# Performance work log

Measured on AMD Instinct MI355X. Metric: run time of the kernel, lower is better.

The kernel has to match this reference:

```python
import jax, jax.numpy as jnp
import numpy as np
import math

B, S, SIG, EMB, LAT, H, L_ENC, L_DEC = 16, 1024, 256, 256, 256, 8, 2, 2
EH, DH = EMB // H, LAT // H
EPS = 1e-10


def _sinusoidal_last_row(d):
    # last row of a standard sinusoidal PE table (position index = max_len-1)
    pos = 5000.0 - 1.0
    i = np.arange(d)
    angles = pos / np.power(10000.0, (2 * (i // 2)) / d)
    pe = np.where(i % 2 == 0, np.sin(angles), np.cos(angles))
    return jnp.asarray(pe, dtype=jnp.float32)


def setup_inputs() -> dict:
    key = jax.random.key(0)
    ks = iter(jax.random.split(key, 64))
    w = lambda *sh: 0.05 * jax.random.normal(next(ks), sh, dtype=jnp.float32)
    z = lambda *sh: jnp.zeros(sh, dtype=jnp.float32)
    d = {
        'inputData': jax.random.normal(next(ks), (B, S, SIG), dtype=jnp.float32),
        'pos_enc': _sinusoidal_last_row(SIG),
        'embW': w(SIG, EMB), 'embb': z(EMB),
        'qW': w(EMB, EMB), 'qb': z(EMB),
        'kW': w(EMB, EMB), 'kb': z(EMB),
        'vW': w(EMB, EMB), 'vb': z(EMB),
        'encBW': w(EH, EH), 'encBb': z(EH),
        'oW': w(EMB, EMB), 'ob': z(EMB),
        'ffe_W1': w(EMB, 2 * EMB), 'ffe_b1': z(2 * EMB),
        'ffe_W2': w(2 * EMB, EMB), 'ffe_b2': z(EMB),
        'lnSA_g': jnp.ones((L_ENC, EMB)), 'lnSA_b': z(L_ENC, EMB),
        'lnFF_g': jnp.ones((L_ENC, EMB)), 'lnFF_b': z(L_ENC, EMB),
        'start': w(1, LAT),
        'decQW': w(LAT, LAT), 'decQb': z(LAT),
        'decKW': w(EMB, EMB), 'decKb': z(EMB),
        'decVW': w(EMB, LAT), 'decVb': z(LAT),
        'decBW': w(EH + DH, DH), 'decBb': z(DH),
        'latW': w(LAT, LAT), 'latb': z(LAT),
        'ffd_W1': w(LAT, LAT // 2), 'ffd_b1': z(LAT // 2),
        'ffd_W2': w(LAT // 2, LAT), 'ffd_b2': z(LAT),
        'lnCA_g': jnp.ones((L_DEC, LAT)), 'lnCA_b': z(L_DEC, LAT),
        'lnLFF_g': jnp.ones((L_DEC, LAT)), 'lnLFF_b': z(L_DEC, LAT),
        'finW': w(LAT, LAT), 'finb': z(LAT),
    }
    return d


def _ln(x, g, b):
    m = x.mean(-1, keepdims=True)
    v = x.var(-1, keepdims=True)
    return (x - m) * jax.lax.rsqrt(v + EPS) * g + b


def _enc_attn(x, qW, qb, kW, kb, vW, vb, bW, bb, oW, ob):
    # x: (B,S,EMB) -> heads (B,H,S,EH)
    sp = lambda t: t.reshape(B, S, H, EH).transpose(0, 2, 1, 3)
    q, k, v = sp(x @ qW + qb), sp(x @ kW + kb), sp(x @ vW + vb)
    bk = k @ bW + bb                                   # bilinear key (B,H,S,EH)
    attn = jax.nn.softmax(jnp.einsum('bhqd,bhkd->bhqk', q, bk) / math.sqrt(EH), axis=-1)
    out = jnp.einsum('bhqk,bhkd->bhqd', attn, v)
    out = out.transpose(0, 2, 1, 3).reshape(B, S, EMB)
    return out @ oW + ob


def _dec_attn(enc, lat, qW, qb, kW, kb, vW, vb, bW, bb, oW, ob):
    # lat: (B,LAT) single query token; enc: (B,S,EMB)
    q = (lat @ qW + qb).reshape(B, 1, H, DH).transpose(0, 2, 1, 3)   # (B,H,1,DH)
    k = (enc @ kW + kb).reshape(B, S, H, EH).transpose(0, 2, 1, 3)   # (B,H,S,EH)
    v = (enc @ vW + vb).reshape(B, S, H, DH).transpose(0, 2, 1, 3)   # (B,H,S,DH)
    qcat = jnp.broadcast_to(q, (B, H, S, DH))
    kcat = jnp.concatenate([k, qcat], axis=-1)                       # (B,H,S,EH+DH)
    bk = kcat @ bW + bb                                              # (B,H,S,DH)
    attn = jax.nn.softmax(jnp.einsum('bhqd,bhkd->bhqk', q, bk) / math.sqrt(EH + DH), axis=-1)
    out = jnp.einsum('bhqk,bhkd->bhqd', attn, v)                     # (B,H,1,DH)
    out = out.transpose(0, 2, 1, 3).reshape(B, LAT)
    return out @ oW + ob


def reference(inputData, pos_enc, embW, embb, qW, qb, kW, kb, vW, vb, encBW, encBb,
              oW, ob, ffe_W1, ffe_b1, ffe_W2, ffe_b2, lnSA_g, lnSA_b, lnFF_g, lnFF_b,
              start, decQW, decQb, decKW, decKb, decVW, decVb, decBW, decBb,
              latW, latb, ffd_W1, ffd_b1, ffd_W2, ffd_b2, lnCA_g, lnCA_b,
              lnLFF_g, lnLFF_b, finW, finb):
    emb = (inputData + pos_enc) @ embW + embb          # (B,S,EMB)
    t = emb
    for l in range(L_ENC):
        n = _ln(t, lnSA_g[l], lnSA_b[l])
        a = _enc_attn(n, qW, qb, kW, kb, vW, vb, encBW, encBb, oW, ob) + n
        t = a + emb
        n2 = _ln(t, lnFF_g[l], lnFF_b[l])
        ff = jax.nn.selu(n2 @ ffe_W1 + ffe_b1) @ ffe_W2 + ffe_b2
        t = ff + n2
    init_lat = jnp.broadcast_to(start, (B, LAT))
    lat = init_lat
    for l in range(L_DEC):
        nl = _ln(init_lat, lnCA_g[l], lnCA_b[l])       # module always feeds initialLatentData
        lat = _dec_attn(t, nl, decQW, decQb, decKW, decKb, decVW, decVb,
                        decBW, decBb, latW, latb)
        nf = _ln(lat, lnLFF_g[l], lnLFF_b[l])
        lat = jax.nn.selu(nf @ ffd_W1 + ffd_b1) @ ffd_W2 + ffd_b2
    return lat @ finW + finb
```

## Files before the change

### kernel.cpp

```cpp
#include <hip/hip_runtime.h>
#include <hip/hip_bf16.h>
#include <math.h>

typedef __hip_bfloat16 bf16;

#define BB 16
#define SS 1024
#define NH 8
#define NR (BB*SS)
#define SZE ((size_t)NR*256)
#define RS 264
#define HS 520

typedef __attribute__((ext_vector_type(8))) short short8;
typedef __attribute__((ext_vector_type(4))) float f32x4;
typedef __attribute__((ext_vector_type(8))) unsigned short u16x8;
typedef __attribute__((ext_vector_type(4))) unsigned short u16x4;

__device__ __forceinline__ float bf2f(bf16 x){ return __bfloat162float(x); }
__device__ __forceinline__ bf16  f2bf(float x){ return __float2bfloat16(x); }
__device__ __forceinline__ unsigned short f2bfu(float x){
  bf16 t = __float2bfloat16(x); return *reinterpret_cast<unsigned short*>(&t);
}
__device__ __forceinline__ float bfu2f(unsigned short u){
  return __uint_as_float(((unsigned)u)<<16);
}

__device__ __forceinline__ float ldT(const float* p, size_t i){ return p[i]; }
__device__ __forceinline__ float ldT(const bf16*  p, size_t i){ return bf2f(p[i]); }
__device__ __forceinline__ void  stT(float* p, size_t i, float v){ p[i] = v; }
__device__ __forceinline__ void  stT(bf16*  p, size_t i, float v){ p[i] = f2bf(v); }

__device__ __forceinline__ float selu_f(float x){
  const float a = 1.6732632423543772f, sc = 1.0507009873554805f;
  return sc * (x > 0.f ? x : a * expm1f(x));
}

__device__ __forceinline__ void gload16(const void* g, void* l){
  __builtin_amdgcn_global_load_lds(
      (const __attribute__((address_space(1))) unsigned int*)g,
      (__attribute__((address_space(3))) unsigned int*)l, 16, 0, 0);
}

struct PtrPack { const void* p[43]; };
struct TabPack { int off[43]; int cnt[43]; int total; };
struct TrTab   { int srcOff[12]; int K[12]; int N[12]; int dstOff[12]; int total; };

__global__ __launch_bounds__(256) void k_canon(PtrPack ptrs, TabPack tab,
    float* __restrict__ dst, int* __restrict__ flagw)
{
  unsigned w0 = ((const unsigned*)ptrs.p[18])[0];
  int isbf = (w0 == 0x3F803F80u) ? 1 : 0;
  if (blockIdx.x == 0 && threadIdx.x == 0) *flagw = isbf;
  __shared__ int so[43], sn[43];
  int tid = threadIdx.x;
  if (tid < 43){ so[tid] = tab.off[tid]; sn[tid] = tab.cnt[tid]; }
  __syncthreads();
  int g = blockIdx.x*256 + tid;
  if (g >= tab.total) return;
  int seg = 1;
  while (seg < 42 && g >= so[seg] + sn[seg]) seg++;
  int li = g - so[seg];
  float v = isbf ? bf2f(((const bf16*)ptrs.p[seg])[li])
                 : ((const float*)ptrs.p[seg])[li];
  dst[g] = v;
}

__global__ __launch_bounds__(256) void k_transW(const float* __restrict__ wt,
    TrTab tt, unsigned short* __restrict__ dst)
{
  int g = blockIdx.x*256 + threadIdx.x;
  if (g >= tt.total) return;
  int seg = 0;
  while (seg < 11 && g >= tt.dstOff[seg] + tt.K[seg]*tt.N[seg]) seg++;
  int li = g - tt.dstOff[seg];
  int K = tt.K[seg], N = tt.N[seg];
  int n = li / K, k = li - n*K;
  dst[g] = f2bfu(wt[tt.srcOff[seg] + (size_t)k*N + n]);
}

__global__ __launch_bounds__(256) void k_qfold(const float* __restrict__ wt,
    int qOff, int qbOff, int bwOff, unsigned short* __restrict__ qW2t,
    float* __restrict__ qbf)
{
  __shared__ float bw[32];
  int n = blockIdx.x, t = threadIdx.x;
  int h = n>>5, d = n&31;
  if (t < 32) bw[t] = wt[bwOff + d*32 + t];
  __syncthreads();
  float acc = 0.f;
  #pragma unroll 8
  for (int j = 0; j < 32; j++) acc += wt[qOff + (size_t)t*256 + h*32 + j]*bw[j];
  qW2t[(size_t)n*256 + t] = f2bfu(acc);
  if (t == 0){
    float a = 0.f;
    #pragma unroll 8
    for (int j = 0; j < 32; j++) a += wt[qbOff + h*32 + j]*bw[j];
    qbf[n] = a;
  }
}

template<int K, int LDA, int CT>
__device__ __forceinline__ void wave_gemmN(const unsigned short (*As)[LDA],
    const unsigned short* __restrict__ Wt, int n0, f32x4 acc[4][CT], int lane)
{
  int col = lane & 15, quad = lane >> 4;
  #pragma unroll
  for (int k0 = 0; k0 < K; k0 += 32){
    short8 a[4], b[CT];
    #pragma unroll
    for (int rt = 0; rt < 4; rt++)
      a[rt] = *(const short8*)(&As[rt*16 + col][k0 + quad*8]);
    #pragma unroll
    for (int ct = 0; ct < CT; ct++)
      b[ct] = *(const short8*)(&Wt[(size_t)(n0 + ct*16 + col)*K + k0 + quad*8]);
    #pragma unroll
    for (int rt = 0; rt < 4; rt++)
      #pragma unroll
      for (int ct = 0; ct < CT; ct++)
        acc[rt][ct] = __builtin_amdgcn_mfma_f32_16x16x32_bf16(a[rt], b[ct], acc[rt][ct], 0, 0, 0);
  }
}

template<int K, int LDA, int CT>
__device__ __forceinline__ void wave_gemmM32(const unsigned short (*As)[LDA],
    const unsigned short* __restrict__ Wt, int n0, f32x4 acc[2][CT], int lane)
{
  int col = lane & 15, quad = lane >> 4;
  #pragma unroll
  for (int k0 = 0; k0 < K; k0 += 32){
    short8 a[2], b[CT];
    #pragma unroll
    for (int rt = 0; rt < 2; rt++)
      a[rt] = *(const short8*)(&As[rt*16 + col][k0 + quad*8]);
    #pragma unroll
    for (int ct = 0; ct < CT; ct++)
      b[ct] = *(const short8*)(&Wt[(size_t)(n0 + ct*16 + col)*K + k0 + quad*8]);
    #pragma unroll
    for (int rt = 0; rt < 2; rt++)
      #pragma unroll
      for (int ct = 0; ct < CT; ct++)
        acc[rt][ct] = __builtin_amdgcn_mfma_f32_16x16x32_bf16(a[rt], b[ct], acc[rt][ct], 0, 0, 0);
  }
}

#define ZERO_ACC4(acc)  { _Pragma("unroll") for (int rt=0;rt<4;rt++){ _Pragma("unroll") for (int ct=0;ct<4;ct++) acc[rt][ct] = (f32x4){0.f,0.f,0.f,0.f}; } }
#define ZERO_ACC2(acc)  { _Pragma("unroll") for (int rt=0;rt<4;rt++){ _Pragma("unroll") for (int ct=0;ct<2;ct++) acc[rt][ct] = (f32x4){0.f,0.f,0.f,0.f}; } }
#define ZERO_ACC24(acc) { _Pragma("unroll") for (int rt=0;rt<2;rt++){ _Pragma("unroll") for (int ct=0;ct<4;ct++) acc[rt][ct] = (f32x4){0.f,0.f,0.f,0.f}; } }

#define EPI_BEGIN(e) { int rt = (e)>>4, ct = ((e)>>2)&3, r = (e)&3; \
    int lrow = rt*16 + quad*4 + r; int gcol0 = ct*16 + col; \
    float av = acc[rt][ct][r]; (void)lrow; (void)gcol0; (void)av;
#define EPI_END }

#define EPI32_BEGIN(e) { int rt = (e)>>4, ct = ((e)>>2)&3, r = (e)&3; \
    int lrow = rt*16 + quad*4 + r; int gcol0 = ct*16 + col; \
    float av = acc[rt][ct][r]; (void)lrow; (void)gcol0; (void)av;
#define EPI32_END }

template<int PRE, typename OT>
__global__ __launch_bounds__(256) void k_gemm_mfma(const void* __restrict__ A,
    const int* __restrict__ flagp, const float* __restrict__ pe,
    const unsigned short* __restrict__ Wt, const float* __restrict__ bias,
    OT* __restrict__ out)
{
  __shared__ __align__(16) unsigned short As[64][RS];
  int tid = threadIdx.x;
  int m = blockIdx.x & 255, nh = blockIdx.x >> 8;
  int row0 = m*64;
  if (PRE == 0){
    int f = *flagp;
    for (int jj = 0; jj < 64; jj++){
      int idx = tid + jj*256, row = idx>>8, c = idx&255;
      size_t g = (size_t)(row0+row)*256 + c;
      float x = f ? bf2f(((const bf16*)A)[g]) : ((const float*)A)[g];
      As[row][c] = f2bfu(x + pe[c]);
    }
  } else {
    for (int jj = 0; jj < 64; jj++){
      int idx = tid + jj*256, row = idx>>8, c = idx&255;
      As[row][c] = f2bfu(((const float*)A)[(size_t)(row0+row)*256 + c]);
    }
  }
  __syncthreads();
  int w = tid>>6, lane = tid&63, col = lane&15, quad = lane>>4;
  int n0 = nh*128 + w*32;
  f32x4 acc[4][2];
  ZERO_ACC2(acc);
  wave_gemmN<256, RS, 2>(As, Wt, n0, acc, lane);
  #pragma unroll
  for (int rt = 0; rt < 4; rt++){
    #pragma unroll
    for (int ct = 0; ct < 2; ct++){
      #pragma unroll
      for (int r = 0; r < 4; r++){
        int grow = row0 + rt*16 + quad*4 + r;
        int gcol = n0 + ct*16 + col;
        stT(out, (size_t)grow*256 + gcol, acc[rt][ct][r] + bias[gcol]);
      }
    }
  }
}

__global__ __launch_bounds__(256) void k_decKV(const float* __restrict__ A,
    const unsigned short* __restrict__ KWt, const float* __restrict__ kb,
    const unsigned short* __restrict__ VWt, const float* __restrict__ vb,
    bf16* __restrict__ ko, bf16* __restrict__ vo)
{
  __shared__ __align__(16) unsigned short As[64][RS];
  int tid = threadIdx.x;
  int m = blockIdx.x & 255, nh = blockIdx.x >> 8;
  int row0 = m*64;
  for (int jj = 0; jj < 64; jj++){
    int idx = tid + jj*256, row = idx>>8, c = idx&255;
    As[row][c] = f2bfu(A[(size_t)(row0+row)*256 + c]);
  }
  __syncthreads();
  int w = tid>>6, lane = tid&63, col = lane&15, quad = lane>>4;
  int n0 = nh*128 + w*32;
  f32x4 acc[4][2];
  ZERO_ACC2(acc);
  wave_gemmN<256, RS, 2>(As, KWt, n0, acc, lane);
  #pragma unroll
  for (int rt = 0; rt < 4; rt++){
    #pragma unroll
    for (int ct = 0; ct < 2; ct++){
      #pragma unroll
      for (int r = 0; r < 4; r++){
        int grow = row0 + rt*16 + quad*4 + r;
        int gcol = n0 + ct*16 + col;
        ko[(size_t)grow*256 + gcol] = f2bf(acc[rt][ct][r] + kb[gcol]);
      }
    }
  }
  ZERO_ACC2(acc);
  wave_gemmN<256, RS, 2>(As, VWt, n0, acc, lane);
  #pragma unroll
  for (int rt = 0; rt < 4; rt++){
    #pragma unroll
    for (int ct = 0; ct < 2; ct++){
      #pragma unroll
      for (int r = 0; r < 4; r++){
        int grow = row0 + rt*16 + quad*4 + r;
        int gcol = n0 + ct*16 + col;
        vo[(size_t)grow*256 + gcol] = f2bf(acc[rt][ct][r] + vb[gcol]);
      }
    }
  }
}

__global__ __launch_bounds__(256) void k_qkvbk_mfma(const float* __restrict__ tsrc,
    const float* __restrict__ lng, const float* __restrict__ lnb,
    const unsigned short* __restrict__ qW2t, const float* __restrict__ qbf,
    const unsigned short* __restrict__ kWt, const float* __restrict__ kb,
    const unsigned short* __restrict__ vWt, const float* __restrict__ vb,
    bf16* __restrict__ qo, bf16* __restrict__ vo, bf16* __restrict__ bko)
{
  __shared__ __align__(16) unsigned short Ns[64][RS];
  __shared__ float mArr[64], rArr[64];
  int tid = threadIdx.x;
  int m = blockIdx.x & 255, nh = blockIdx.x >> 8;
  int row0 = m*64;
  int b = row0 >> 10, s0 = row0 & 1023;
  {
    int row = tid>>2, l4 = tid&3;
    const float* rp = tsrc + (size_t)(row0+row)*256;
    float s = 0.f, s2 = 0.f;
    for (int c = l4; c < 256; c += 4){ float x = rp[c]; s += x; s2 += x*x; }
    s  += __shfl_down(s, 2, 4);  s  += __shfl_down(s, 1, 4);
    s2 += __shfl_down(s2, 2, 4); s2 += __shfl_down(s2, 1, 4);
    if (l4 == 0){
      float mn = s*(1.f/256.f);
      float v = s2*(1.f/256.f) - mn*mn;
      mArr[row] = mn; rArr[row] = rsqrtf(fmaxf(v,0.f) + 1e-10f);
    }
  }
  __syncthreads();
  for (int jj = 0; jj < 64; jj++){
    int idx = tid + jj*256, row = idx>>8, c = idx&255;
    float x = tsrc[(size_t)(row0+row)*256 + c];
    Ns[row][c] = f2bfu((x - mArr[row])*rArr[row]*lng[c] + lnb[c]);
  }
  __syncthreads();
  int w = tid>>6, lane = tid&63, col = lane&15, quad = lane>>4;
  int n0 = nh*128 + w*32;
  f32x4 acc[4][2];
  ZERO_ACC2(acc);
  wave_gemmN<256, RS, 2>(Ns, qW2t, n0, acc, lane);
  #pragma unroll
  for (int rt = 0; rt < 4; rt++){
    #pragma unroll
    for (int ct = 0; ct < 2; ct++){
      #pragma unroll
      for (int r = 0; r < 4; r++){
        int grow = row0 + rt*16 + quad*4 + r;
        int gcol = n0 + ct*16 + col;
        qo[(size_t)grow*256 + gcol] = f2bf(acc[rt][ct][r] + qbf[gcol]);
      }
    }
  }
  ZERO_ACC2(acc);
  wave_gemmN<256, RS, 2>(Ns, vWt, n0, acc, lane);
  #pragma unroll
  for (int rt = 0; rt < 4; rt++){
    #pragma unroll
    for (int ct = 0; ct < 2; ct++){
      #pragma unroll
      for (int r = 0; r < 4; r++){
        int grow = row0 + rt*16 + quad*4 + r;
        int gcol = n0 + ct*16 + col;
        vo[(size_t)grow*256 + gcol] = f2bf(acc[rt][ct][r] + vb[gcol]);
      }
    }
  }
  ZERO_ACC2(acc);
  wave_gemmN<256, RS, 2>(Ns, kWt, n0, acc, lane);
  int h = nh*4 + w;
  #pragma unroll
  for (int rt = 0; rt < 4; rt++){
    #pragma unroll
    for (int ct = 0; ct < 2; ct++){
      #pragma unroll
      for (int r = 0; r < 4; r++){
        int srow = s0 + rt*16 + quad*4 + r;
        int d = ct*16 + col;
        bko[(((size_t)(b*NH+h))*SS + srow)*32 + d] =
            f2bf(acc[rt][ct][r] + kb[h*32 + d]);
      }
    }
  }
}

__global__ __launch_bounds__(256) void k_attn_mfma(
    const bf16* __restrict__ q, const bf16* __restrict__ bk,
    const bf16* __restrict__ v, bf16* __restrict__ ao)
{
  int bi = blockIdx.x;
  int qq = bi >> 7, b = (bi >> 3) & 15, h = bi & 7;
  int tid = threadIdx.x;
  int w = tid>>6, lane = tid&63;
  int quad = lane>>4, col = lane&15;
  int q0 = qq*128 + w*32;

  __shared__ __align__(16) unsigned short Ks2b[2][64][32];
  __shared__ __align__(16) unsigned short Vt2b[2][32][76];
  __shared__ __align__(16) unsigned short Ps[4][32][68];

  const float scale2 = 0.17677669529663687f * 1.4426950408889634f;
  short8 aq[2];
  #pragma unroll
  for (int rt = 0; rt < 2; rt++){
    const unsigned short* gq = (const unsigned short*)q
        + ((size_t)(b*SS + q0 + rt*16 + col))*256 + h*32 + quad*8;
    u16x8 qv = *(const u16x8*)gq;
    #pragma unroll
    for (int i=0;i<8;i++) aq[rt][i] = (short)f2bfu(bfu2f(qv[i])*scale2);
  }

  float l_r[2][4];
  f32x4 o0[2], o1[2];
  #pragma unroll
  for (int rt=0;rt<2;rt++){
    o0[rt] = (f32x4){0.f,0.f,0.f,0.f};
    o1[rt] = (f32x4){0.f,0.f,0.f,0.f};
    #pragma unroll
    for (int r=0;r<4;r++) l_r[rt][r] = 0.f;
  }

  int krow = tid>>2, ksl = tid&3;
  int kslw = ksl ^ ((krow>>1)&3);
  int vk0 = tid>>3, vdg = tid&7;
  int vk1 = vk0 + 32;
  int rsl = (quad ^ ((col>>1)&3))*8;

  const unsigned short* bkp = (const unsigned short*)bk + ((size_t)(b*NH+h))*SS*32;
  const unsigned short* vp  = (const unsigned short*)v + (size_t)b*SS*256 + h*32;

  u16x8 rK;
  u16x4 rV0, rV1;
  {
    rK  = *(const u16x8*)(bkp + (size_t)krow*32 + ksl*8);
    rV0 = *(const u16x4*)(vp + (size_t)vk0*256 + vdg*4);
    rV1 = *(const u16x4*)(vp + (size_t)vk1*256 + vdg*4);
  }

  for (int kt = 0; kt < 16; kt++){
    int cb = kt & 1;
    *(u16x8*)(&Ks2b[cb][krow][kslw*8]) = rK;
    #pragma unroll
    for (int i=0;i<4;i++) Vt2b[cb][vdg*4+i][vk0] = rV0[i];
    #pragma unroll
    for (int i=0;i<4;i++) Vt2b[cb][vdg*4+i][vk1] = rV1[i];
    __syncthreads();
    if (kt < 15){
      int nk = kt + 1;
      rK  = *(const u16x8*)(bkp + (size_t)(nk*64 + krow)*32 + ksl*8);
      rV0 = *(const u16x4*)(vp + (size_t)(nk*64 + vk0)*256 + vdg*4);
      rV1 = *(const u16x4*)(vp + (size_t)(nk*64 + vk1)*256 + vdg*4);
    }
    short8 bk8[4];
    #pragma unroll
    for (int t4 = 0; t4 < 4; t4++)
      bk8[t4] = *(const short8*)(&Ks2b[cb][t4*16 + col][rsl]);
    #pragma unroll
    for (int rt = 0; rt < 2; rt++){
      f32x4 s[4];
      #pragma unroll
      for (int t4 = 0; t4 < 4; t4++)
        s[t4] = __builtin_amdgcn_mfma_f32_16x16x32_bf16(aq[rt], bk8[t4],
                  (f32x4){0.f,0.f,0.f,0.f}, 0, 0, 0);
      #pragma unroll
      for (int r=0;r<4;r++){
        #pragma unroll
        for (int t4=0;t4<4;t4++){
          float pv = __builtin_amdgcn_exp2f(s[t4][r]);
          l_r[rt][r] += pv;
          Ps[w][rt*16 + quad*4 + r][t4*16 + col] =
              (unsigned short)(__float_as_uint(pv) >> 16);
        }
      }
    }
    short8 bv00 = *(const short8*)(&Vt2b[cb][col][quad*8]);
    short8 bv10 = *(const short8*)(&Vt2b[cb][col][32 + quad*8]);
    short8 bv01 = *(const short8*)(&Vt2b[cb][16+col][quad*8]);
    short8 bv11 = *(const short8*)(&Vt2b[cb][16+col][32 + quad*8]);
    #pragma unroll
    for (int rt = 0; rt < 2; rt++){
      short8 ap0 = *(const short8*)(&Ps[w][rt*16 + col][quad*8]);
      short8 ap1 = *(const short8*)(&Ps[w][rt*16 + col][32 + quad*8]);
      o0[rt] = __builtin_amdgcn_mfma_f32_16x16x32_bf16(ap0, bv00, o0[rt], 0, 0, 0);
      o0[rt] = __builtin_amdgcn_mfma_f32_16x16x32_bf16(ap1, bv10, o0[rt], 0, 0, 0);
      o1[rt] = __builtin_amdgcn_mfma_f32_16x16x32_bf16(ap0, bv01, o1[rt], 0, 0, 0);
      o1[rt] = __builtin_amdgcn_mfma_f32_16x16x32_bf16(ap1, bv11, o1[rt], 0, 0, 0);
    }
  }
  #pragma unroll
  for (int rt=0;rt<2;rt++){
    #pragma unroll
    for (int r=0;r<4;r++){
      float l = l_r[rt][r];
      #pragma unroll
      for (int msk=1; msk<16; msk<<=1) l += __shfl_xor(l, msk, 64);
      float inv = 1.f / l;
      int qrow = q0 + rt*16 + quad*4 + r;
      size_t o = ((size_t)(b*SS + qrow))*256 + h*32;
      ao[o + col]      = f2bf(o0[rt][r]*inv);
      ao[o + 16 + col] = f2bf(o1[rt][r]*inv);
    }
  }
}

__global__ __launch_bounds__(256) void k_oln_mfma(
    const float* __restrict__ tsrc, const float* __restrict__ emb,
    const bf16* __restrict__ ao,
    const float* __restrict__ lnSAg, const float* __restrict__ lnSAb,
    const unsigned short* __restrict__ oWt, const float* __restrict__ ob,
    const float* __restrict__ lnFFg, const float* __restrict__ lnFFb,
    bf16* __restrict__ n2o)
{
  __shared__ __align__(16) unsigned short Aos[32][RS];
  __shared__ __align__(16) unsigned short Tm[32][RS];
  __shared__ float mArr[32], rArr[32];
  int tid = threadIdx.x, row0 = blockIdx.x*32;
  {
    int row = tid>>3, l8 = tid&7;
    const float* rp = tsrc + (size_t)(row0+row)*256;
    float s = 0.f, s2 = 0.f;
    for (int c = l8; c < 256; c += 8){ float x = rp[c]; s += x; s2 += x*x; }
    s  += __shfl_down(s, 4, 8);  s  += __shfl_down(s, 2, 8);  s  += __shfl_down(s, 1, 8);
    s2 += __shfl_down(s2, 4, 8); s2 += __shfl_down(s2, 2, 8); s2 += __shfl_down(s2, 1, 8);
    if (l8 == 0){
      float m = s*(1.f/256.f);
      float v = s2*(1.f/256.f) - m*m;
      mArr[row] = m; rArr[row] = rsqrtf(fmaxf(v,0.f) + 1e-10f);
    }
  }
  for (int jj = 0; jj < 4; jj++){
    int idx = tid + jj*256;
    int row = idx>>5, c8 = idx&31;
    *(u16x8*)(&Aos[row][c8*8]) =
        *(const u16x8*)((const unsigned short*)ao + (size_t)(row0+row)*256 + c8*8);
  }
  __syncthreads();
  int w = tid>>6, lane = tid&63, col = lane&15, quad = lane>>4;
  f32x4 acc[2][4];
  ZERO_ACC24(acc);
  wave_gemmM32<256, RS, 4>(Aos, oWt, w*64, acc, lane);
  #pragma unroll
  for (int e = 0; e < 32; e++){
    EPI32_BEGIN(e)
    int gcol = w*64 + gcol0;
    size_t g = (size_t)(row0+lrow)*256 + gcol;
    float n1 = (tsrc[g] - mArr[lrow])*rArr[lrow]*lnSAg[gcol] + lnSAb[gcol];
    Tm[lrow][gcol] = f2bfu(av + ob[gcol] + n1 + emb[g]);
    EPI32_END
  }
  __syncthreads();
  {
    int row = tid>>3, l8 = tid&7;
    float s = 0.f, s2 = 0.f;
    for (int c = l8; c < 256; c += 8){ float x = bfu2f(Tm[row][c]); s += x; s2 += x*x; }
    s  += __shfl_down(s, 4, 8);  s  += __shfl_down(s, 2, 8);  s  += __shfl_down(s, 1, 8);
    s2 += __shfl_down(s2, 4, 8); s2 += __shfl_down(s2, 2, 8); s2 += __shfl_down(s2, 1, 8);
    if (l8 == 0){
      float m = s*(1.f/256.f);
      float v = s2*(1.f/256.f) - m*m;
      mArr[row] = m; rArr[row] = rsqrtf(fmaxf(v,0.f) + 1e-10f);
    }
  }
  __syncthreads();
  for (int jj = 0; jj < 32; jj++){
    int idx = tid + jj*256, row = idx>>8, c = idx&255;
    float x = bfu2f(Tm[row][c]);
    n2o[(size_t)(row0+row)*256 + c] =
        f2bf((x - mArr[row])*rArr[row]*lnFFg[c] + lnFFb[c]);
  }
}

#define FF_STAGE(B, KT) { \
  int k0 = (KT)*64; \
  _Pragma("unroll") \
  for (int i = 0; i < 4; i++){ int c = w*4 + i; \
    gload16(A  + (size_t)(row0 + c*8 + rsub)*KFULL + k0 + sgo, &As[B][c*512]); } \
  _Pragma("unroll") \
  for (int i = 0; i < 2; i++){ int c = w*2 + i; \
    gload16(Wb + (size_t)(n0   + c*8 + rsub)*KFULL + k0 + sgo, &Bs[B][c*512]); } }

#define FF_COMPUTE(B) { \
  _Pragma("unroll") \
  for (int kk = 0; kk < 2; kk++){ \
    short8 a[4], b2r[2]; \
    _Pragma("unroll") \
    for (int rt = 0; rt < 4; rt++) \
      a[rt] = *(const short8*)(&As[B][((wr*64 + rt*16 + col)<<6) + ((((kk<<2)|quad) ^ (col&7))<<3)]); \
    _Pragma("unroll") \
    for (int ct = 0; ct < 2; ct++) \
      b2r[ct] = *(const short8*)(&Bs[B][((wc*32 + ct*16 + col)<<6) + ((((kk<<2)|quad) ^ (col&7))<<3)]); \
    _Pragma("unroll") \
    for (int rt = 0; rt < 4; rt++) \
      _Pragma("unroll") \
      for (int ct = 0; ct < 2; ct++) \
        acc[rt][ct] = __builtin_amdgcn_mfma_f32_16x16x32_bf16(a[rt], b2r[ct], acc[rt][ct], 0, 0, 0); } }

template<int KFULL, int NFULL, int EPI>
__global__ __launch_bounds__(256) void k_ff_gemm(const bf16* __restrict__ A,
    const unsigned short* __restrict__ Wt, const float* __restrict__ bias,
    const bf16* __restrict__ res, void* __restrict__ outv)
{
  __shared__ __align__(16) unsigned short As[2][128*64];
  __shared__ __align__(16) unsigned short Bs[2][64*64];
  constexpr int NWG = 128 * (NFULL/64);
  constexpr int NKT = KFULL/64;
  int tid = threadIdx.x;
  int w = tid>>6, lane = tid&63;
  int col = lane&15, quad = lane>>4;
  int wr = w>>1, wc = w&1;
  int rsub = lane>>3;
  int sgo = (((lane&7) ^ rsub)<<3);
  int bid = blockIdx.x;
  int swz = (bid & 7)*(NWG>>3) + (bid >> 3);
  int mb = swz & 127, nb = swz >> 7;
  int row0 = mb*128, n0 = nb*64;
  const bf16* Wb = (const bf16*)Wt;

  f32x4 acc[4][2];
  ZERO_ACC2(acc);

  FF_STAGE(0, 0);
  __syncthreads();
  #pragma unroll
  for (int kt = 0; kt < NKT-1; kt++){
    int cb = kt & 1;
    FF_STAGE(cb^1, kt+1);
    FF_COMPUTE(cb);
    __syncthreads();
  }
  FF_COMPUTE((NKT-1)&1);

  if (EPI == 0){
    bf16* o = (bf16*)outv;
    #pragma unroll
    for (int rt = 0; rt < 4; rt++){
      #pragma unroll
      for (int ct = 0; ct < 2; ct++){
        #pragma unroll
        for (int r = 0; r < 4; r++){
          int grow = row0 + wr*64 + rt*16 + quad*4 + r;
          int gcol = n0 + wc*32 + ct*16 + col;
          o[(size_t)grow*NFULL + gcol] = f2bf(selu_f(acc[rt][ct][r] + bias[gcol]));
        }
      }
    }
  } else {
    float* o = (float*)outv;
    #pragma unroll
    for (int rt = 0; rt < 4; rt++){
      #pragma unroll
      for (int ct = 0; ct < 2; ct++){
        #pragma unroll
        for (int r = 0; r < 4; r++){
          int grow = row0 + wr*64 + rt*16 + quad*4 + r;
          int gcol = n0 + wc*32 + ct*16 + col;
          size_t g = (size_t)grow*NFULL + gcol;
          o[g] = acc[rt][ct][r] + bias[gcol] + bf2f(res[g]);
        }
      }
    }
  }
}

__global__ __launch_bounds__(256) void k_dec_head(const float* __restrict__ startp,
    const float* __restrict__ lng, const float* __restrict__ lnb,
    const float* __restrict__ decQW, const float* __restrict__ decQb,
    const float* __restrict__ decBW,
    float* __restrict__ s_q, float* __restrict__ s_qc)
{
  __shared__ float s1[256], s2[256], nl[256], qv[256];
  int t = threadIdx.x;
  float v = startp[t];
  s1[t]=v; s2[t]=v*v; __syncthreads();
  for (int s=128;s>0;s>>=1){
    if (t<s){ s1[t]+=s1[t+s]; s2[t]+=s2[t+s]; }
    __syncthreads();
  }
  float m = s1[0]*(1.f/256.f);
  float var = s2[0]*(1.f/256.f) - m*m;
  float r = rsqrtf(fmaxf(var,0.f) + 1e-10f);
  nl[t] = (v-m)*r*lng[t] + lnb[t];
  __syncthreads();
  float acc = decQb[t];
  for (int k=0;k<256;k++) acc += nl[k]*decQW[k*256+t];
  qv[t] = acc; s_q[t] = acc;
  __syncthreads();
  int h = t>>5, d = t&31;
  float a = 0.f;
  #pragma unroll 8
  for (int e=0;e<32;e++) a += qv[h*32+e]*decBW[(32+e)*32 + d];
  s_qc[t] = a;
}

__global__ __launch_bounds__(256) void k_bkdec_mfma(const bf16* __restrict__ kk,
    const float* __restrict__ qc, const unsigned short* __restrict__ decBWt,
    const float* __restrict__ Bb, bf16* __restrict__ bko)
{
  __shared__ __align__(16) unsigned short Ks[64][RS];
  int tid = threadIdx.x, row0 = blockIdx.x*64;
  int b = row0 >> 10, s0 = row0 & 1023;
  for (int jj = 0; jj < 8; jj++){
    int idx = tid + jj*256;
    int row = idx>>5, c8 = idx&31;
    *(u16x8*)(&Ks[row][c8*8]) =
        *(const u16x8*)((const unsigned short*)kk + (size_t)(row0+row)*256 + c8*8);
  }
  __syncthreads();
  int w = tid>>6, lane = tid&63, col = lane&15, quad = lane>>4;
  f32x4 acc[4][4];
  ZERO_ACC4(acc);
  #pragma unroll
  for (int ct = 0; ct < 4; ct++){
    int base = w*64 + ct*16;
    int h = base >> 5, d0 = base & 31;
    short8 bfrag = *(const short8*)(&decBWt[(size_t)(d0 + col)*32 + quad*8]);
    #pragma unroll
    for (int rt = 0; rt < 4; rt++){
      short8 afrag = *(const short8*)(&Ks[rt*16 + col][h*32 + quad*8]);
      acc[rt][ct] = __builtin_amdgcn_mfma_f32_16x16x32_bf16(afrag, bfrag, acc[rt][ct], 0, 0, 0);
    }
  }
  #pragma unroll
  for (int e = 0; e < 64; e++){
    EPI_BEGIN(e)
    int srow = s0 + lrow;
    int gcol = w*64 + gcol0;
    int h = gcol >> 5, d = gcol & 31;
    bko[(((size_t)(b*NH+h))*SS + srow)*32 + d] = f2bf(av + qc[gcol] + Bb[d]);
    EPI_END
  }
}

__global__ __launch_bounds__(256) void k_attn_dec(const float* __restrict__ q,
    const bf16* __restrict__ bk, const bf16* __restrict__ v,
    float* __restrict__ out)
{
  int h = blockIdx.x & 7, b = blockIdx.x >> 3;
  int tid = threadIdx.x;
  __shared__ float qs[32];
  __shared__ float sc[SS];
  __shared__ float red[256];
  if (tid < 32) qs[tid] = q[h*32 + tid] * (0.125f * 1.4426950408889634f);
  __syncthreads();
  float lsum = 0.f;
  for (int jj=0;jj<4;jj++){
    int j = tid*4 + jj;
    size_t base = (((size_t)(b*NH+h))*SS + j)*32;
    float s = 0.f;
    #pragma unroll
    for (int d=0;d<32;d++) s += qs[d]*bf2f(bk[base + d]);
    float e = __builtin_amdgcn_exp2f(s);
    sc[j] = e; lsum += e;
  }
  red[tid] = lsum; __syncthreads();
  for (int s=128;s>0;s>>=1){ if (tid<s) red[tid]+=red[tid+s]; __syncthreads(); }
  float gs = red[0];
  __syncthreads();
  int d = tid & 31, c = tid >> 5;
  float acc = 0.f;
  for (int j=c*128; j<c*128+128; j++)
    acc += sc[j]*bf2f(v[((size_t)(b*SS + j))*256 + h*32 + d]);
  red[c*32+d] = acc;
  __syncthreads();
  if (tid < 32){
    float s = 0.f;
    #pragma unroll
    for (int cc=0;cc<8;cc++) s += red[cc*32+tid];
    out[b*256 + h*32 + tid] = s / gs;
  }
}

__global__ __launch_bounds__(256) void k_dec_tail(const float* __restrict__ s_ao,
    const float* __restrict__ latW, const float* __restrict__ latb,
    const float* __restrict__ lng, const float* __restrict__ lnb,
    const float* __restrict__ W1, const float* __restrict__ b1,
    const float* __restrict__ W2, const float* __restrict__ b2,
    const float* __restrict__ finW, const float* __restrict__ finb,
    const int* __restrict__ flagp, void* __restrict__ outv)
{
  __shared__ float x[256], y[256], s1[256], s2[256];
  int t = threadIdx.x, b = blockIdx.x;
  x[t] = s_ao[b*256 + t];
  __syncthreads();
  float lat = latb[t];
  for (int k=0;k<256;k++) lat += x[k]*latW[k*256+t];
  s1[t]=lat; s2[t]=lat*lat; __syncthreads();
  for (int s=128;s>0;s>>=1){
    if (t<s){ s1[t]+=s1[t+s]; s2[t]+=s2[t+s]; }
    __syncthreads();
  }
  float m = s1[0]*(1.f/256.f);
  float var = s2[0]*(1.f/256.f) - m*m;
  float r = rsqrtf(fmaxf(var,0.f) + 1e-10f);
  y[t] = (lat-m)*r*lng[t] + lnb[t];
  __syncthreads();
  if (t < 128){
    float a2 = b1[t];
    for (int k=0;k<256;k++) a2 += y[k]*W1[k*128+t];
    x[t] = selu_f(a2);
  }
  __syncthreads();
  float a3 = b2[t];
  for (int k=0;k<128;k++) a3 += x[k]*W2[k*256+t];
  s1[t] = a3;
  __syncthreads();
  float o = finb[t];
  for (int k=0;k<256;k++) o += s1[k]*finW[k*256+t];
  size_t oi = (size_t)b*256 + t;
  if (*flagp) ((bf16*)outv)[oi] = f2bf(o);
  else        ((float*)outv)[oi] = o;
}

extern "C" void kernel_launch(void* const* d_in, const int* in_sizes, int n_in,
                              void* d_out, int out_size, void* d_ws, size_t ws_size,
                              hipStream_t stream)
{
  static const int cnts[43] = {
    0,256,65536,256,65536,256,65536,256,65536,256,1024,32,65536,256,
    131072,512,131072,256,512,512,512,512,256,65536,256,65536,256,65536,256,
    2048,32,65536,256,32768,128,32768,256,512,512,512,512,65536,256 };
  TabPack tab; int acc0 = 0;
  for (int i = 0; i < 43; i++){ tab.off[i] = acc0; tab.cnt[i] = cnts[i]; acc0 += cnts[i]; }
  tab.total = acc0;
  PtrPack ptrs;
  for (int i = 0; i < 43; i++) ptrs.p[i] = d_in[i];

  char* p = (char*)d_ws;
  float* wt   = (float*)p;
  int*  flagp = (int*)(p + (4u<<20));
  char* bigc  = p + (4u<<20) + 256;
  float* g_emb = (float*)bigc;
  float* g_t   = (float*)(bigc + SZE*4);
  bf16*  g_q   = (bf16*)(bigc + 2*SZE*4);
  bf16*  g_v   = (bf16*)(bigc + 2*SZE*4 + SZE*2);
  bf16*  g_ao  = (bf16*)(bigc + 2*SZE*4 + 2*SZE*2);
  bf16*  g_bk  = (bf16*)(bigc + 2*SZE*4 + 3*SZE*2);
  float* fsm   = (float*)(bigc + 2*SZE*4 + 4*SZE*2);
  unsigned short* wtr = (unsigned short*)(bigc + 2*SZE*4 + 4*SZE*2 + 131072*4);
  float* s_q  = fsm;
  float* s_qc = fsm + 256;
  float* s_ao = fsm + 512;
  float* qbf  = fsm + 8192;
  bf16*  g_h1 = g_v;

  static const int trIdx[10] = {2,4,6,8,12,14,16,25,27,10};
  static const int trK[10]   = {256,256,256,256,256,256,512,256,256,32};
  static const int trN[10]   = {256,256,256,256,256,512,256,256,256,32};
  TrTab tr; int tacc = 0;
  for (int i = 0; i < 10; i++){
    tr.srcOff[i] = tab.off[trIdx[i]];
    tr.K[i] = trK[i]; tr.N[i] = trN[i];
    tr.dstOff[i] = tacc; tacc += trK[i]*trN[i];
  }
  tr.srcOff[10] = tab.off[29];        tr.K[10]=32; tr.N[10]=32; tr.dstOff[10]=tacc; tacc+=1024;
  tr.srcOff[11] = tab.off[29] + 1024; tr.K[11]=32; tr.N[11]=32; tr.dstOff[11]=tacc; tacc+=1024;
  tr.total = tacc;
  const unsigned short *embWt = wtr + tr.dstOff[0],
    *kWt = wtr + tr.dstOff[2], *vWt = wtr + tr.dstOff[3], *oWt = wtr + tr.dstOff[4],
    *ffeW1t = wtr + tr.dstOff[5], *ffeW2t = wtr + tr.dstOff[6],
    *decKWt = wtr + tr.dstOff[7], *decVWt = wtr + tr.dstOff[8],
    *decBWtk = wtr + tr.dstOff[10];
  unsigned short* qW2t = wtr + tr.total;

  #define WP(i) (wt + tab.off[i])
  const float *pe=WP(1), *embb=WP(3), *qb=WP(5), *kb=WP(7), *vb=WP(9),
    *ob=WP(13), *ffeb1=WP(15), *ffeb2=WP(17),
    *lnSAg=WP(18), *lnSAb=WP(19), *lnFFg=WP(20), *lnFFb=WP(21),
    *startp=WP(22), *decQW=WP(23), *decQb=WP(24), *decKb=WP(26),
    *decVb=WP(28), *decBW=WP(29), *decBb=WP(30), *latW=WP(31),
    *latb=WP(32), *ffdW1=WP(33), *ffdb1=WP(34), *ffdW2=WP(35), *ffdb2=WP(36),
    *lnCAg=WP(37), *lnCAb=WP(38), *lnLFFg=WP(39), *lnLFFb=WP(40),
    *finW=WP(41), *finb=WP(42);

  dim3 blk(256);
  const int G64  = NR/64;
  const int G32  = NR/32;
  const int GSP  = 512;
  const int GA2  = 1024;
  const int LD   = 1;

  k_canon<<<(tab.total+255)/256, blk, 0, stream>>>(ptrs, tab, wt, flagp);
  k_transW<<<(tr.total+255)/256, blk, 0, stream>>>(wt, tr, wtr);
  k_qfold<<<256, blk, 0, stream>>>(wt, tab.off[4], tab.off[5], tab.off[10], qW2t, qbf);

  k_gemm_mfma<0,float><<<GSP, blk, 0, stream>>>(d_in[0], flagp, pe, embWt, embb, g_emb);

  const float* tcur = g_emb;
  for (int l = 0; l < 2; l++){
    k_qkvbk_mfma<<<GSP, blk, 0, stream>>>(tcur, lnSAg+l*256, lnSAb+l*256,
        qW2t, qbf, kWt, kb, vWt, vb, g_q, g_v, g_bk);
    k_attn_mfma<<<GA2, blk, 0, stream>>>(g_q, g_bk, g_v, g_ao);
    k_oln_mfma<<<G32, blk, 0, stream>>>(tcur, g_emb, g_ao,
        lnSAg+l*256, lnSAb+l*256, oWt, ob, lnFFg+l*256, lnFFb+l*256, g_q);
    k_ff_gemm<256,512,0><<<1024, blk, 0, stream>>>(g_q, ffeW1t, ffeb1, (const bf16*)nullptr, g_h1);
    k_ff_gemm<512,256,1><<<512, blk, 0, stream>>>(g_h1, ffeW2t, ffeb2, g_q, g_t);
    tcur = g_t;
  }

  k_dec_head<<<1, blk, 0, stream>>>(startp, lnCAg+LD*256, lnCAb+LD*256,
      decQW, decQb, decBW, s_q, s_qc);
  k_decKV<<<GSP, blk, 0, stream>>>(g_t, decKWt, decKb, decVWt, decVb, g_q, g_v);
  k_bkdec_mfma<<<G64, blk, 0, stream>>>(g_q, s_qc, decBWtk, decBb, g_bk);
  k_attn_dec<<<BB*NH, blk, 0, stream>>>(s_q, g_bk, g_v, s_ao);
  k_dec_tail<<<BB, blk, 0, stream>>>(s_ao, latW, latb, lnLFFg+LD*256, lnLFFb+LD*256,
      ffdW1, ffdb1, ffdW2, ffdb2, finW, finb, flagp, d_out);
  #undef WP
}
```

Measured before the change: 522.8 us.

## Software-pipeline attention QK with softmax/PV and vectorize GEMM A-tile loads

Restructures the attention loop so the QK MFMAs for tile k+1 are issued before the exp/PV work of tile k, using two score register sets and a triple-buffered V tile in LDS to keep the one-sync-per-tile schedule safe. Separately, the fp32 row loads in the GEMM, decKV and LN+QKV kernels are vectorized to float4 with packed 4-wide bf16 LDS stores, and the LayerNorm stats loop reads float4. The pipelining raises register pressure (extra score accumulators) and LDS use, which could reduce occupancy.

```diff
diff --git a/kernel.cpp b/kernel.cpp
--- a/kernel.cpp
+++ b/kernel.cpp
@@ -177,9 +177,11 @@
       As[row][c] = f2bfu(x + pe[c]);
     }
   } else {
-    for (int jj = 0; jj < 64; jj++){
-      int idx = tid + jj*256, row = idx>>8, c = idx&255;
-      As[row][c] = f2bfu(((const float*)A)[(size_t)(row0+row)*256 + c]);
+    for (int jj = 0; jj < 16; jj++){
+      int idx = tid + jj*256;
+      int row = idx>>6, c4 = (idx&63)<<2;
+      float4 x = *(const float4*)((const float*)A + (size_t)(row0+row)*256 + c4);
+      *(u16x4*)(&As[row][c4]) = (u16x4){f2bfu(x.x),f2bfu(x.y),f2bfu(x.z),f2bfu(x.w)};
     }
   }
   __syncthreads();
@@ -211,9 +213,11 @@
   int tid = threadIdx.x;
   int m = blockIdx.x & 255, nh = blockIdx.x >> 8;
   int row0 = m*64;
-  for (int jj = 0; jj < 64; jj++){
-    int idx = tid + jj*256, row = idx>>8, c = idx&255;
-    As[row][c] = f2bfu(A[(size_t)(row0+row)*256 + c]);
+  for (int jj = 0; jj < 16; jj++){
+    int idx = tid + jj*256;
+    int row = idx>>6, c4 = (idx&63)<<2;
+    float4 x = *(const float4*)(A + (size_t)(row0+row)*256 + c4);
+    *(u16x4*)(&As[row][c4]) = (u16x4){f2bfu(x.x),f2bfu(x.y),f2bfu(x.z),f2bfu(x.w)};
   }
   __syncthreads();
   int w = tid>>6, lane = tid&63, col = lane&15, quad = lane>>4;
@@ -264,9 +268,14 @@
   int b = row0 >> 10, s0 = row0 & 1023;
   {
     int row = tid>>2, l4 = tid&3;
-    const float* rp = tsrc + (size_t)(row0+row)*256;
+    const float4* rp = (const float4*)(tsrc + (size_t)(row0+row)*256) + l4*16;
     float s = 0.f, s2 = 0.f;
-    for (int c = l4; c < 256; c += 4){ float x = rp[c]; s += x; s2 += x*x; }
+    #pragma unroll 4
+    for (int c = 0; c < 16; c++){
+      float4 x = rp[c];
+      s += x.x + x.y + x.z + x.w;
+      s2 += x.x*x.x + x.y*x.y + x.z*x.z + x.w*x.w;
+    }
     s  += __shfl_down(s, 2, 4);  s  += __shfl_down(s, 1, 4);
     s2 += __shfl_down(s2, 2, 4); s2 += __shfl_down(s2, 1, 4);
     if (l4 == 0){
@@ -276,10 +285,17 @@
     }
   }
   __syncthreads();
-  for (int jj = 0; jj < 64; jj++){
-    int idx = tid + jj*256, row = idx>>8, c = idx&255;
-    float x = tsrc[(size_t)(row0+row)*256 + c];
-    Ns[row][c] = f2bfu((x - mArr[row])*rArr[row]*lng[c] + lnb[c]);
+  for (int jj = 0; jj < 16; jj++){
+    int idx = tid + jj*256;
+    int row = idx>>6, c4 = (idx&63)<<2;
+    float4 x = *(const float4*)(tsrc + (size_t)(row0+row)*256 + c4);
+    float mn = mArr[row], rr = rArr[row];
+    u16x4 o;
+    o[0] = f2bfu((x.x - mn)*rr*lng[c4+0] + lnb[c4+0]);
+    o[1] = f2bfu((x.y - mn)*rr*lng[c4+1] + lnb[c4+1]);
+    o[2] = f2bfu((x.z - mn)*rr*lng[c4+2] + lnb[c4+2]);
+    o[3] = f2bfu((x.w - mn)*rr*lng[c4+3] + lnb[c4+3]);
+    *(u16x4*)(&Ns[row][c4]) = o;
   }
   __syncthreads();
   int w = tid>>6, lane = tid&63, col = lane&15, quad = lane>>4;
@@ -331,6 +347,56 @@
   }
 }
 
+#define AT_STAGE(KT) { \
+  int cb=(KT)&1, vb=(KT)%3; \
+  *(u16x8*)(&Ks2b[cb][krow][kslw*8]) = rK; \
+  _Pragma("unroll") for (int i=0;i<4;i++) Vt3b[vb][vdg*4+i][vk0] = rV0[i]; \
+  _Pragma("unroll") for (int i=0;i<4;i++) Vt3b[vb][vdg*4+i][vk1] = rV1[i]; }
+
+#define AT_PREF(KT) { \
+  rK  = *(const u16x8*)(bkp + (size_t)((KT)*64 + krow)*32 + ksl*8); \
+  rV0 = *(const u16x4*)(vp + (size_t)((KT)*64 + vk0)*256 + vdg*4); \
+  rV1 = *(const u16x4*)(vp + (size_t)((KT)*64 + vk1)*256 + vdg*4); }
+
+#define AT_QK(KT, S) { \
+  int cb=(KT)&1; \
+  short8 bk8[4]; \
+  _Pragma("unroll") \
+  for (int t4=0;t4<4;t4++) bk8[t4] = *(const short8*)(&Ks2b[cb][t4*16+col][rsl]); \
+  _Pragma("unroll") \
+  for (int rt=0;rt<2;rt++){ \
+    _Pragma("unroll") \
+    for (int t4=0;t4<4;t4++) \
+      S[rt][t4] = __builtin_amdgcn_mfma_f32_16x16x32_bf16(aq[rt], bk8[t4], \
+                    (f32x4){0.f,0.f,0.f,0.f}, 0, 0, 0); } }
+
+#define AT_FINISH(KT, S) { \
+  int vb=(KT)%3; \
+  _Pragma("unroll") \
+  for (int rt=0;rt<2;rt++){ \
+    _Pragma("unroll") \
+    for (int r=0;r<4;r++){ \
+      _Pragma("unroll") \
+      for (int t4=0;t4<4;t4++){ \
+        float pv = __builtin_amdgcn_exp2f(S[rt][t4][r]); \
+        l_r[rt][r] += pv; \
+        Ps[w][rt*16 + quad*4 + r][t4*16 + col] = \
+            (unsigned short)(__float_as_uint(pv) >> 16); \
+      } } } \
+  short8 bv00 = *(const short8*)(&Vt3b[vb][col][quad*8]); \
+  short8 bv10 = *(const short8*)(&Vt3b[vb][col][32 + quad*8]); \
+  short8 bv01 = *(const short8*)(&Vt3b[vb][16+col][quad*8]); \
+  short8 bv11 = *(const short8*)(&Vt3b[vb][16+col][32 + quad*8]); \
+  _Pragma("unroll") \
+  for (int rt=0;rt<2;rt++){ \
+    short8 ap0 = *(const short8*)(&Ps[w][rt*16 + col][quad*8]); \
+    short8 ap1 = *(const short8*)(&Ps[w][rt*16 + col][32 + quad*8]); \
+    o0[rt] = __builtin_amdgcn_mfma_f32_16x16x32_bf16(ap0, bv00, o0[rt], 0, 0, 0); \
+    o0[rt] = __builtin_amdgcn_mfma_f32_16x16x32_bf16(ap1, bv10, o0[rt], 0, 0, 0); \
+    o1[rt] = __builtin_amdgcn_mfma_f32_16x16x32_bf16(ap0, bv01, o1[rt], 0, 0, 0); \
+    o1[rt] = __builtin_amdgcn_mfma_f32_16x16x32_bf16(ap1, bv11, o1[rt], 0, 0, 0); \
+  } }
+
 __global__ __launch_bounds__(256) void k_attn_mfma(
     const bf16* __restrict__ q, const bf16* __restrict__ bk,
     const bf16* __restrict__ v, bf16* __restrict__ ao)
@@ -343,7 +409,7 @@
   int q0 = qq*128 + w*32;
 
   __shared__ __align__(16) unsigned short Ks2b[2][64][32];
-  __shared__ __align__(16) unsigned short Vt2b[2][32][76];
+  __shared__ __align__(16) unsigned short Vt3b[3][32][76];
   __shared__ __align__(16) unsigned short Ps[4][32][68];
 
   const float scale2 = 0.17677669529663687f * 1.4426950408889634f;
@@ -378,62 +444,26 @@
 
   u16x8 rK;
   u16x4 rV0, rV1;
-  {
-    rK  = *(const u16x8*)(bkp + (size_t)krow*32 + ksl*8);
-    rV0 = *(const u16x4*)(vp + (size_t)vk0*256 + vdg*4);
-    rV1 = *(const u16x4*)(vp + (size_t)vk1*256 + vdg*4);
-  }
-
-  for (int kt = 0; kt < 16; kt++){
-    int cb = kt & 1;
-    *(u16x8*)(&Ks2b[cb][krow][kslw*8]) = rK;
-    #pragma unroll
-    for (int i=0;i<4;i++) Vt2b[cb][vdg*4+i][vk0] = rV0[i];
-    #pragma unroll
-    for (int i=0;i<4;i++) Vt2b[cb][vdg*4+i][vk1] = rV1[i];
-    __syncthreads();
-    if (kt < 15){
-      int nk = kt + 1;
-      rK  = *(const u16x8*)(bkp + (size_t)(nk*64 + krow)*32 + ksl*8);
-      rV0 = *(const u16x4*)(vp + (size_t)(nk*64 + vk0)*256 + vdg*4);
-      rV1 = *(const u16x4*)(vp + (size_t)(nk*64 + vk1)*256 + vdg*4);
-    }
-    short8 bk8[4];
-    #pragma unroll
-    for (int t4 = 0; t4 < 4; t4++)
-      bk8[t4] = *(const short8*)(&Ks2b[cb][t4*16 + col][rsl]);
-    #pragma unroll
-    for (int rt = 0; rt < 2; rt++){
-      f32x4 s[4];
-      #pragma unroll
-      for (int t4 = 0; t4 < 4; t4++)
-        s[t4] = __builtin_amdgcn_mfma_f32_16x16x32_bf16(aq[rt], bk8[t4],
-                  (f32x4){0.f,0.f,0.f,0.f}, 0, 0, 0);
-      #pragma unroll
-      for (int r=0;r<4;r++){
-        #pragma unroll
-        for (int t4=0;t4<4;t4++){
-          float pv = __builtin_amdgcn_exp2f(s[t4][r]);
-          l_r[rt][r] += pv;
-          Ps[w][rt*16 + quad*4 + r][t4*16 + col] =
-              (unsigned short)(__float_as_uint(pv) >> 16);
-        }
-      }
-    }
-    short8 bv00 = *(const short8*)(&Vt2b[cb][col][quad*8]);
-    short8 bv10 = *(const short8*)(&Vt2b[cb][col][32 + quad*8]);
-    short8 bv01 = *(const short8*)(&Vt2b[cb][16+col][quad*8]);
-    short8 bv11 = *(const short8*)(&Vt2b[cb][16+col][32 + quad*8]);
-    #pragma unroll
-    for (int rt = 0; rt < 2; rt++){
-      short8 ap0 = *(const short8*)(&Ps[w][rt*16 + col][quad*8]);
-      short8 ap1 = *(const short8*)(&Ps[w][rt*16 + col][32 + quad*8]);
-      o0[rt] = __builtin_amdgcn_mfma_f32_16x16x32_bf16(ap0, bv00, o0[rt], 0, 0, 0);
-      o0[rt] = __builtin_amdgcn_mfma_f32_16x16x32_bf16(ap1, bv10, o0[rt], 0, 0, 0);
-      o1[rt] = __builtin_amdgcn_mfma_f32_16x16x32_bf16(ap0, bv01, o1[rt], 0, 0, 0);
-      o1[rt] = __builtin_amdgcn_mfma_f32_16x16x32_bf16(ap1, bv11, o1[rt], 0, 0, 0);
-    }
-  }
+  AT_PREF(0);
+
+  f32x4 sA[2][4], sB[2][4];
+
+  AT_STAGE(0); __syncthreads(); AT_PREF(1);
+  AT_QK(0, sA);
+  for (int t = 0; t < 7; ++t){
+    int k1 = 2*t+1, k2 = 2*t+2;
+    AT_STAGE(k1); __syncthreads(); AT_PREF(k1+1);
+    AT_QK(k1, sB);
+    AT_FINISH(k1-1, sA);
+    AT_STAGE(k2); __syncthreads(); AT_PREF(k2+1);
+    AT_QK(k2, sA);
+    AT_FINISH(k1, sB);
+  }
+  AT_STAGE(15); __syncthreads();
+  AT_QK(15, sB);
+  AT_FINISH(14, sA);
+  AT_FINISH(15, sB);
+
   #pragma unroll
   for (int rt=0;rt<2;rt++){
     #pragma unroll
```

Result: no change. 527.4 us (+0.9%).

## Keep softmax probabilities in registers via transposed MFMA and vectorize row loads

Applied to the files above, without the earlier changes.

The attention kernel now computes S^T by swapping MFMA operands, so each lane holds four consecutive key scores for one query. These are packed to bf16 with v_perm and fed straight into the PV MFMA as the B operand, which removes the per-wave LDS staging buffer for P along with its scattered writes and reads. Output is accumulated transposed and stored as 4-wide vectors, and the row sum now needs only two cross-lane shuffles. Separately, the fp32-to-bf16 LDS staging loops and the LayerNorm statistics loops in the GEMM kernels use float4 loads instead of scalar loads.

```diff
diff --git a/kernel.cpp b/kernel.cpp
--- a/kernel.cpp
+++ b/kernel.cpp
@@ -177,9 +177,11 @@
       As[row][c] = f2bfu(x + pe[c]);
     }
   } else {
-    for (int jj = 0; jj < 64; jj++){
-      int idx = tid + jj*256, row = idx>>8, c = idx&255;
-      As[row][c] = f2bfu(((const float*)A)[(size_t)(row0+row)*256 + c]);
+    for (int jj = 0; jj < 16; jj++){
+      int idx = tid + jj*256;
+      int row = idx>>6, c4 = (idx&63)<<2;
+      float4 x = *(const float4*)((const float*)A + (size_t)(row0+row)*256 + c4);
+      *(u16x4*)(&As[row][c4]) = (u16x4){f2bfu(x.x),f2bfu(x.y),f2bfu(x.z),f2bfu(x.w)};
     }
   }
   __syncthreads();
@@ -211,9 +213,11 @@
   int tid = threadIdx.x;
   int m = blockIdx.x & 255, nh = blockIdx.x >> 8;
   int row0 = m*64;
-  for (int jj = 0; jj < 64; jj++){
-    int idx = tid + jj*256, row = idx>>8, c = idx&255;
-    As[row][c] = f2bfu(A[(size_t)(row0+row)*256 + c]);
+  for (int jj = 0; jj < 16; jj++){
+    int idx = tid + jj*256;
+    int row = idx>>6, c4 = (idx&63)<<2;
+    float4 x = *(const float4*)(A + (size_t)(row0+row)*256 + c4);
+    *(u16x4*)(&As[row][c4]) = (u16x4){f2bfu(x.x),f2bfu(x.y),f2bfu(x.z),f2bfu(x.w)};
   }
   __syncthreads();
   int w = tid>>6, lane = tid&63, col = lane&15, quad = lane>>4;
@@ -264,9 +268,14 @@
   int b = row0 >> 10, s0 = row0 & 1023;
   {
     int row = tid>>2, l4 = tid&3;
-    const float* rp = tsrc + (size_t)(row0+row)*256;
+    const float4* rp = (const float4*)(tsrc + (size_t)(row0+row)*256) + l4*16;
     float s = 0.f, s2 = 0.f;
-    for (int c = l4; c < 256; c += 4){ float x = rp[c]; s += x; s2 += x*x; }
+    #pragma unroll 4
+    for (int c = 0; c < 16; c++){
+      float4 x = rp[c];
+      s += x.x + x.y + x.z + x.w;
+      s2 += x.x*x.x + x.y*x.y + x.z*x.z + x.w*x.w;
+    }
     s  += __shfl_down(s, 2, 4);  s  += __shfl_down(s, 1, 4);
     s2 += __shfl_down(s2, 2, 4); s2 += __shfl_down(s2, 1, 4);
     if (l4 == 0){
@@ -276,10 +285,17 @@
     }
   }
   __syncthreads();
-  for (int jj = 0; jj < 64; jj++){
-    int idx = tid + jj*256, row = idx>>8, c = idx&255;
-    float x = tsrc[(size_t)(row0+row)*256 + c];
-    Ns[row][c] = f2bfu((x - mArr[row])*rArr[row]*lng[c] + lnb[c]);
+  for (int jj = 0; jj < 16; jj++){
+    int idx = tid + jj*256;
+    int row = idx>>6, c4 = (idx&63)<<2;
+    float4 x = *(const float4*)(tsrc + (size_t)(row0+row)*256 + c4);
+    float mn = mArr[row], rr = rArr[row];
+    u16x4 o;
+    o[0] = f2bfu((x.x - mn)*rr*lng[c4+0] + lnb[c4+0]);
+    o[1] = f2bfu((x.y - mn)*rr*lng[c4+1] + lnb[c4+1]);
+    o[2] = f2bfu((x.z - mn)*rr*lng[c4+2] + lnb[c4+2]);
+    o[3] = f2bfu((x.w - mn)*rr*lng[c4+3] + lnb[c4+3]);
+    *(u16x4*)(&Ns[row][c4]) = o;
   }
   __syncthreads();
   int w = tid>>6, lane = tid&63, col = lane&15, quad = lane>>4;
@@ -344,7 +360,6 @@
 
   __shared__ __align__(16) unsigned short Ks2b[2][64][32];
   __shared__ __align__(16) unsigned short Vt2b[2][32][76];
-  __shared__ __align__(16) unsigned short Ps[4][32][68];
 
   const float scale2 = 0.17677669529663687f * 1.4426950408889634f;
   short8 aq[2];
@@ -357,15 +372,12 @@
     for (int i=0;i<8;i++) aq[rt][i] = (short)f2bfu(bfu2f(qv[i])*scale2);
   }
 
-  float l_r[2][4];
-  f32x4 o0[2], o1[2];
-  #pragma unroll
-  for (int rt=0;rt<2;rt++){
-    o0[rt] = (f32x4){0.f,0.f,0.f,0.f};
-    o1[rt] = (f32x4){0.f,0.f,0.f,0.f};
-    #pragma unroll
-    for (int r=0;r<4;r++) l_r[rt][r] = 0.f;
-  }
+  float l_r[2] = {0.f, 0.f};
+  f32x4 o[2][2];
+  #pragma unroll
+  for (int rt=0;rt<2;rt++)
+    #pragma unroll
+    for (int ct=0;ct<2;ct++) o[rt][ct] = (f32x4){0.f,0.f,0.f,0.f};
 
   int krow = tid>>2, ksl = tid&3;
   int kslw = ksl ^ ((krow>>1)&3);
@@ -378,11 +390,9 @@
 
   u16x8 rK;
   u16x4 rV0, rV1;
-  {
-    rK  = *(const u16x8*)(bkp + (size_t)krow*32 + ksl*8);
-    rV0 = *(const u16x4*)(vp + (size_t)vk0*256 + vdg*4);
-    rV1 = *(const u16x4*)(vp + (size_t)vk1*256 + vdg*4);
-  }
+  rK  = *(const u16x8*)(bkp + (size_t)krow*32 + ksl*8);
+  rV0 = *(const u16x4*)(vp + (size_t)vk0*256 + vdg*4);
+  rV1 = *(const u16x4*)(vp + (size_t)vk1*256 + vdg*4);
 
   for (int kt = 0; kt < 16; kt++){
     int cb = kt & 1;
@@ -398,54 +408,62 @@
       rV0 = *(const u16x4*)(vp + (size_t)(nk*64 + vk0)*256 + vdg*4);
       rV1 = *(const u16x4*)(vp + (size_t)(nk*64 + vk1)*256 + vdg*4);
     }
-    short8 bk8[4];
-    #pragma unroll
-    for (int t4 = 0; t4 < 4; t4++)
-      bk8[t4] = *(const short8*)(&Ks2b[cb][t4*16 + col][rsl]);
-    #pragma unroll
-    for (int rt = 0; rt < 2; rt++){
-      f32x4 s[4];
-      #pragma unroll
-      for (int t4 = 0; t4 < 4; t4++)
-        s[t4] = __builtin_amdgcn_mfma_f32_16x16x32_bf16(aq[rt], bk8[t4],
-                  (f32x4){0.f,0.f,0.f,0.f}, 0, 0, 0);
-      #pragma unroll
-      for (int r=0;r<4;r++){
+    #pragma unroll
+    for (int g = 0; g < 2; g++){
+      unsigned pk[2][4];
+      #pragma unroll
+      for (int tt = 0; tt < 2; tt++){
+        int t4 = g*2 + tt;
+        short8 bk8 = *(const short8*)(&Ks2b[cb][t4*16 + col][rsl]);
         #pragma unroll
-        for (int t4=0;t4<4;t4++){
-          float pv = __builtin_amdgcn_exp2f(s[t4][r]);
-          l_r[rt][r] += pv;
-          Ps[w][rt*16 + quad*4 + r][t4*16 + col] =
-              (unsigned short)(__float_as_uint(pv) >> 16);
+        for (int rt = 0; rt < 2; rt++){
+          f32x4 s = __builtin_amdgcn_mfma_f32_16x16x32_bf16(bk8, aq[rt],
+                      (f32x4){0.f,0.f,0.f,0.f}, 0, 0, 0);
+          float e0 = __builtin_amdgcn_exp2f(s[0]);
+          float e1 = __builtin_amdgcn_exp2f(s[1]);
+          float e2 = __builtin_amdgcn_exp2f(s[2]);
+          float e3 = __builtin_amdgcn_exp2f(s[3]);
+          l_r[rt] += (e0+e1)+(e2+e3);
+          pk[rt][tt*2+0] = __builtin_amdgcn_perm(
+              __float_as_uint(e1), __float_as_uint(e0), 0x07060302u);
+          pk[rt][tt*2+1] = __builtin_amdgcn_perm(
+              __float_as_uint(e3), __float_as_uint(e2), 0x07060302u);
         }
       }
-    }
-    short8 bv00 = *(const short8*)(&Vt2b[cb][col][quad*8]);
-    short8 bv10 = *(const short8*)(&Vt2b[cb][col][32 + quad*8]);
-    short8 bv01 = *(const short8*)(&Vt2b[cb][16+col][quad*8]);
-    short8 bv11 = *(const short8*)(&Vt2b[cb][16+col][32 + quad*8]);
-    #pragma unroll
-    for (int rt = 0; rt < 2; rt++){
-      short8 ap0 = *(const short8*)(&Ps[w][rt*16 + col][quad*8]);
-      short8 ap1 = *(const short8*)(&Ps[w][rt*16 + col][32 + quad*8]);
-      o0[rt] = __builtin_amdgcn_mfma_f32_16x16x32_bf16(ap0, bv00, o0[rt], 0, 0, 0);
-      o0[rt] = __builtin_amdgcn_mfma_f32_16x16x32_bf16(ap1, bv10, o0[rt], 0, 0, 0);
-      o1[rt] = __builtin_amdgcn_mfma_f32_16x16x32_bf16(ap0, bv01, o1[rt], 0, 0, 0);
-      o1[rt] = __builtin_amdgcn_mfma_f32_16x16x32_bf16(ap1, bv11, o1[rt], 0, 0, 0);
+      short8 av[2];
+      #pragma unroll
+      for (int ct = 0; ct < 2; ct++){
+        u16x4 v0 = *(const u16x4*)(&Vt2b[cb][ct*16+col][(g*2+0)*16 + quad*4]);
+        u16x4 v1 = *(const u16x4*)(&Vt2b[cb][ct*16+col][(g*2+1)*16 + quad*4]);
+        av[ct][0]=(short)v0[0]; av[ct][1]=(short)v0[1];
+        av[ct][2]=(short)v0[2]; av[ct][3]=(short)v0[3];
+        av[ct][4]=(short)v1[0]; av[ct][5]=(short)v1[1];
+        av[ct][6]=(short)v1[2]; av[ct][7]=(short)v1[3];
+      }
+      #pragma unroll
+      for (int rt = 0; rt < 2; rt++){
+        union { unsigned u[4]; short8 s8; } pb;
+        pb.u[0]=pk[rt][0]; pb.u[1]=pk[rt][1]; pb.u[2]=pk[rt][2]; pb.u[3]=pk[rt][3];
+        #pragma unroll
+        for (int ct = 0; ct < 2; ct++)
+          o[rt][ct] = __builtin_amdgcn_mfma_f32_16x16x32_bf16(
+              av[ct], pb.s8, o[rt][ct], 0, 0, 0);
+      }
     }
   }
   #pragma unroll
   for (int rt=0;rt<2;rt++){
-    #pragma unroll
-    for (int r=0;r<4;r++){
-      float l = l_r[rt][r];
-      #pragma unroll
-      for (int msk=1; msk<16; msk<<=1) l += __shfl_xor(l, msk, 64);
-      float inv = 1.f / l;
-      int qrow = q0 + rt*16 + quad*4 + r;
-      size_t o = ((size_t)(b*SS + qrow))*256 + h*32;
-      ao[o + col]      = f2bf(o0[rt][r]*inv);
-      ao[o + 16 + col] = f2bf(o1[rt][r]*inv);
+    float l = l_r[rt];
+    l += __shfl_xor(l, 16, 64);
+    l += __shfl_xor(l, 32, 64);
+    float inv = 1.f / l;
+    size_t obase = ((size_t)(b*SS + q0 + rt*16 + col))*256 + h*32;
+    #pragma unroll
+    for (int ct=0;ct<2;ct++){
+      u16x4 ov;
+      #pragma unroll
+      for (int r=0;r<4;r++) ov[r] = f2bfu(o[rt][ct][r]*inv);
+      *(u16x4*)((unsigned short*)ao + obase + ct*16 + quad*4) = ov;
     }
   }
 }
```

After: 501.0 us. 1.04x faster.
